# Optimization experiments

Hardware: AMD Instinct MI355X
Metric: run time of the kernel (lower is better)

## Reference

```python
import jax, jax.numpy as jnp
import numpy as np
from jax import lax

N, CIN, COUT, T, V = 32, 64, 128, 256, 25
IC = COUT // 4
EPS = 1e-5


def setup_inputs() -> dict:
    key = jax.random.key(0)
    ks = jax.random.split(key, 16)
    rn = lambda k, shape, s=0.05: jax.random.normal(k, shape, jnp.float32) * s
    inp = {
        'x': jax.random.normal(ks[0], (N, CIN, T, V), jnp.float32),
        'A': rn(ks[1], (V, V), 0.2),
        'w1': rn(ks[2], (IC, CIN)), 'b1': rn(ks[3], (IC,), 0.01),
        'w2': rn(ks[4], (IC, CIN)), 'b2': rn(ks[5], (IC,), 0.01),
        'w3': rn(ks[6], (COUT, CIN)), 'b3': rn(ks[7], (COUT,), 0.01),
        'w4': rn(ks[8], (COUT, CIN)), 'b4': rn(ks[9], (COUT,), 0.01),
        'bn1_g': jnp.ones((COUT,)), 'bn1_b': jnp.zeros((COUT,)),
        'bn1_m': rn(ks[10], (COUT,), 0.1), 'bn1_v': jnp.ones((COUT,)),
        'wt': rn(ks[11], (COUT, COUT, 9, 1)), 'bt': rn(ks[12], (COUT,), 0.01),
        'bn2_g': jnp.ones((COUT,)), 'bn2_b': jnp.zeros((COUT,)),
        'bn2_m': rn(ks[13], (COUT,), 0.1), 'bn2_v': jnp.ones((COUT,)),
        'wr': rn(ks[14], (COUT, CIN)), 'br': rn(ks[15], (COUT,), 0.01),
        'bnr_g': jnp.ones((COUT,)), 'bnr_b': jnp.zeros((COUT,)),
        'bnr_m': jnp.zeros((COUT,)), 'bnr_v': jnp.ones((COUT,)),
    }
    return inp


def _conv1x1(x, w, b):
    # 1x1 Conv2d over (T,V): pure channel mix. x: [N,C,T,V], w: [O,C]
    return jnp.einsum('oc,nctv->notv', w, x) + b[None, :, None, None]


def _bn(x, g, b, m, v):
    # BatchNorm2d in eval mode (running stats)
    scale = g / jnp.sqrt(v + EPS)
    return x * scale[None, :, None, None] + (b - m * scale)[None, :, None, None]


def _forward(x, A, w1, b1, w2, b2, w3, b3, w4, b4,
             bn1_g, bn1_b, bn1_m, bn1_v, wt, bt,
             bn2_g, bn2_b, bn2_m, bn2_v, wr, br,
             bnr_g, bnr_b, bnr_m, bnr_v):
    n, _, t, v = x.shape
    cout = w3.shape[0]
    ic = cout // 4
    x1 = _conv1x1(x, w1, b1).mean(axis=2)  # [N,IC,V]
    x2 = _conv1x1(x, w2, b2).mean(axis=2)  # [N,IC,V]
    a = jax.nn.softmax(x1[..., :, None] - x2[..., None, :], axis=-1)  # [N,IC,V,V]
    x3 = _conv1x1(x, w3, b3).reshape(n, 4, ic, t, v)
    y = jnp.einsum('ncuv,nmctv->nmctu', a, x3).reshape(n, cout, t, v)
    y = y + jnp.einsum('uv,nctv->nctu', A, _conv1x1(x, w4, b4))
    # tcn: BN -> ReLU -> Conv2d (9,1) pad (4,0) -> BN
    y = jax.nn.relu(_bn(y, bn1_g, bn1_b, bn1_m, bn1_v))
    y = lax.conv_general_dilated(
        y, wt, window_strides=(1, 1), padding=[(4, 4), (0, 0)],
        dimension_numbers=('NCHW', 'OIHW', 'NCHW')) + bt[None, :, None, None]
    y = _bn(y, bn2_g, bn2_b, bn2_m, bn2_v)
    # residual branch (in_channels != out_channels): 1x1 conv + BN
    res = _bn(_conv1x1(x, wr, br), bnr_g, bnr_b, bnr_m, bnr_v)
    return jax.nn.relu(y + res)


def reference(x, A, w1, b1, w2, b2, w3, b3, w4, b4,
              bn1_g, bn1_b, bn1_m, bn1_v, wt, bt,
              bn2_g, bn2_b, bn2_m, bn2_v, wr, br,
              bnr_g, bnr_b, bnr_m, bnr_v):
    return _forward(x, A, w1, b1, w2, b2, w3, b3, w4, b4,
                    bn1_g, bn1_b, bn1_m, bn1_v, wt, bt,
                    bn2_g, bn2_b, bn2_m, bn2_v, wr, br,
                    bnr_g, bnr_b, bnr_m, bnr_v)
```

## Files before the change

kernel.cpp:

```cpp
#include <hip/hip_runtime.h>
#include <hip/hip_bf16.h>

typedef unsigned short u16;
typedef unsigned int u32;
typedef unsigned long long u64;
typedef __attribute__((ext_vector_type(8))) short short8;
typedef __attribute__((ext_vector_type(4))) float f32x4;

#define DI __device__ __forceinline__

DI float b2f(u16 v){ u32 u = ((u32)v) << 16; float f; __builtin_memcpy(&f, &u, 4); return f; }
DI u16 f2bu(float f){ __hip_bfloat16 h = __float2bfloat16(f); u16 u; __builtin_memcpy(&u, &h, 2); return u; }

DI void gll16(const u16* g, u16* l){
  __builtin_amdgcn_global_load_lds((const __attribute__((address_space(1))) void*)g,
                                   (__attribute__((address_space(3))) void*)l, 16, 0, 0);
}

__global__ __launch_bounds__(256) void kprep(const float* __restrict__ x, u16* __restrict__ xT){
  __shared__ u16 tile[128*72];
  const int xb = blockIdx.x, n = blockIdx.y, tid = threadIdx.x;
  const int x0 = xb*128;
  const int ci = tid>>2, part = tid&3;
  const float* src = x + ((size_t)(n*64+ci))*6400 + x0 + part*32;
  #pragma unroll
  for (int i=0;i<8;i++){
    float4 f = ((const float4*)src)[i];
    const int col = part*32 + i*4;
    tile[(col+0)*72+ci] = f2bu(f.x);
    tile[(col+1)*72+ci] = f2bu(f.y);
    tile[(col+2)*72+ci] = f2bu(f.z);
    tile[(col+3)*72+ci] = f2bu(f.w);
  }
  __syncthreads();
  const int row = tid>>1, half = tid&1;
  short8* dst = (short8*)(xT + ((size_t)n*6400 + x0 + row)*64 + half*32);
  const short8* s8 = (const short8*)(tile + row*72 + half*32);
  #pragma unroll
  for (int i=0;i<4;i++) dst[i] = s8[i];
}

__global__ __launch_bounds__(256) void kzero(float* __restrict__ xm){
  const int i = blockIdx.x*1024 + threadIdx.x*4;
  float4 z = {0.f,0.f,0.f,0.f};
  *(float4*)(xm + i) = z;
}

__global__ __launch_bounds__(256) void kmean(const u16* __restrict__ xT, float* __restrict__ xm){
  __shared__ float part[4][1600];
  const int seg = blockIdx.x, n = blockIdx.y, tid = threadIdx.x;
  const int tg = tid>>6, c = tid&63;
  float acc[25];
  #pragma unroll
  for (int v=0;v<25;v++) acc[v]=0.f;
  for (int t = seg*32 + tg; t < seg*32 + 32; t += 4){
    const u16* base = xT + ((size_t)n*6400 + t*25)*64 + c;
    #pragma unroll
    for (int v=0;v<25;v++) acc[v] += b2f(base[v*64]);
  }
  #pragma unroll
  for (int v=0;v<25;v++) part[tg][v*64+c] = acc[v];
  __syncthreads();
  for (int idx = tid; idx < 1600; idx += 256){
    const int v = idx>>6, cc = idx&63;
    const float m = part[0][idx]+part[1][idx]+part[2][idx]+part[3][idx];
    atomicAdd(&xm[(n*64+cc)*25+v], m*(1.f/256.f));
  }
}

__global__ __launch_bounds__(64) void kp(const float* __restrict__ xm, const float* __restrict__ w2,
                                         const float* __restrict__ b2p, const float* __restrict__ Ab,
                                         float* __restrict__ p, float* __restrict__ rsA){
  const int c = blockIdx.x, n = blockIdx.y, lane = threadIdx.x;
  __shared__ float sc[32];
  __shared__ float red[2];
  float neg = 0.f;
  if (lane < 25){
    float acc = b2p[c];
    for (int k = 0; k < 64; k++) acc += w2[c*64 + k] * xm[(n*64 + k)*25 + lane];
    neg = -acc;
    sc[lane] = neg;
  }
  __syncthreads();
  if (lane == 0){
    float m = sc[0];
    for (int i = 1; i < 25; i++) m = fmaxf(m, sc[i]);
    red[0] = m;
  }
  __syncthreads();
  float e = 0.f;
  if (lane < 25){ e = expf(neg - red[0]); sc[lane] = e; }
  __syncthreads();
  if (lane == 0){
    float ssum = 0.f;
    for (int i = 0; i < 25; i++) ssum += sc[i];
    red[1] = ssum;
  }
  __syncthreads();
  if (lane < 25) p[(n*32 + c)*25 + lane] = e / red[1];
  if (n == 0 && c == 0 && lane < 25){
    float r = 0.f;
    for (int v = 0; v < 25; v++) r += Ab[lane*25 + v];
    rsA[lane] = r;
  }
}

__global__ __launch_bounds__(256) void kxa(const u16* __restrict__ xT, const float* __restrict__ Ab,
                                           u16* __restrict__ xA){
  __shared__ float xl[200*68];
  __shared__ float al[625];
  const int tc = blockIdx.x, n = blockIdx.y, tid = threadIdx.x;
  const int x0t = tc * 200;
  for (int i = tid; i < 625; i += 256) al[i] = Ab[i];
  for (int idx = tid; idx < 1600; idx += 256){
    const int r = idx>>3, i = idx&7;
    short8 v = *(const short8*)(xT + ((size_t)n*6400 + x0t + r)*64 + i*8);
    float* dst = xl + r*68 + i*8;
    #pragma unroll
    for (int e=0;e<8;e++) dst[e] = b2f((u16)v[e]);
  }
  __syncthreads();
  if (tid < 200){
    const int t_ = tid / 25, u = tid % 25;
    float acc[64];
    #pragma unroll
    for (int k = 0; k < 64; k++) acc[k] = 0.f;
    const float* arow = al + u*25;
    for (int v = 0; v < 25; v++){
      const float a = arow[v];
      const float* xr = xl + (t_*25 + v)*68;
      #pragma unroll
      for (int k = 0; k < 64; k++) acc[k] += a * xr[k];
    }
    u16* dst = xA + ((size_t)n*6400 + x0t + tid)*64;
    #pragma unroll
    for (int k = 0; k < 64; k += 4){
      u64 pk = (u64)f2bu(acc[k]) | ((u64)f2bu(acc[k+1])<<16)
             | ((u64)f2bu(acc[k+2])<<32) | ((u64)f2bu(acc[k+3])<<48);
      *(u64*)(dst + k) = pk;
    }
  }
}

__global__ __launch_bounds__(256) void kwt(const float* __restrict__ wt, u16* __restrict__ wtb){
  const int o = blockIdx.x*256 + threadIdx.x;
  const int dt = o >> 14, rem = o & 16383;
  wtb[o] = f2bu(wt[rem*9 + dt]);
}

__global__ __launch_bounds__(256) void kwr(const float* __restrict__ wrw, const float* __restrict__ g2,
      const float* __restrict__ v2, const float* __restrict__ gr, const float* __restrict__ vr,
      const float* __restrict__ w3, const float* __restrict__ w4,
      const float* __restrict__ bt, const float* __restrict__ bb2, const float* __restrict__ m2,
      const float* __restrict__ bbr, const float* __restrict__ mr, const float* __restrict__ brb,
      u16* __restrict__ wrb, u16* __restrict__ w3b, u16* __restrict__ w4b,
      float* __restrict__ e0, float* __restrict__ e1){
  const int b = blockIdx.x, tid = threadIdx.x;
  if (b < 32){
    const int o = b*256 + tid;
    const int co = o >> 6;
    const float E0 = g2[co]*rsqrtf(v2[co]+1e-5f);
    const float R0 = gr[co]*rsqrtf(vr[co]+1e-5f);
    wrb[o] = f2bu(wrw[o]*R0/E0);
  } else if (b < 64){
    const int o = (b-32)*256 + tid;
    w3b[o] = f2bu(w3[o]);
  } else if (b < 96){
    const int o = (b-64)*256 + tid;
    w4b[o] = f2bu(w4[o]);
  } else if (tid < 128){
    const float scv2 = g2[tid]*rsqrtf(v2[tid]+1e-5f);
    const float scvr = gr[tid]*rsqrtf(vr[tid]+1e-5f);
    e0[tid] = scv2;
    e1[tid] = scv2*bt[tid] + bb2[tid] - m2[tid]*scv2
            + (bbr[tid] - mr[tid]*scvr + scvr*brb[tid]);
  }
}

__global__ __launch_bounds__(256) void khpad(u16* __restrict__ h){
  const int n = blockIdx.x, side = blockIdx.y, tid = threadIdx.x;
  short8* base = (short8*)(h + ((size_t)n*6600 + (side ? 6500 : 0))*128);
  short8 z = {0,0,0,0,0,0,0,0};
  for (int i = tid; i < 1600; i += 256) base[i] = z;
}

__global__ __launch_bounds__(256) void ks(const u16* __restrict__ xT, const u16* __restrict__ w3b,
                                          const float* __restrict__ p, float* __restrict__ s){
  __shared__ __align__(16) char smem[53248];
  __shared__ float pL[800];
  u16* aL = (u16*)smem;
  u16* bL = (u16*)(smem + 18432);
  float* z3 = (float*)smem;
  const int xb = blockIdx.x, n = blockIdx.y, tid = threadIdx.x;
  const int x0 = xb*100, t0 = xb*4;
  const int row = tid >> 1, half = tid & 1;
  {
    short8* dst = (short8*)(aL + row*72 + half*32);
    const short8* src = (const short8*)(w3b + row*64 + half*32);
    #pragma unroll
    for (int i=0;i<4;i++) dst[i] = src[i];
  }
  {
    short8* dst = (short8*)(bL + row*72 + half*32);
    if (row < 100){
      const short8* src = (const short8*)(xT + ((size_t)n*6400 + x0 + row)*64 + half*32);
      #pragma unroll
      for (int i=0;i<4;i++) dst[i] = src[i];
    } else {
      short8 z = {0,0,0,0,0,0,0,0};
      #pragma unroll
      for (int i=0;i<4;i++) dst[i] = z;
    }
  }
  for (int i = tid; i < 800; i += 256) pL[i] = p[n*800 + i];
  __syncthreads();
  const int wave = tid>>6, lane = tid&63, q = lane>>4, l = lane&15;
  const int wr = wave>>1, wc = wave&1;
  f32x4 acc[4][4];
  #pragma unroll
  for (int i=0;i<4;i++)
    #pragma unroll
    for (int j=0;j<4;j++){ f32x4 z0 = {0.f,0.f,0.f,0.f}; acc[i][j] = z0; }
  #pragma unroll
  for (int ksi = 0; ksi < 2; ksi++){
    const int kb = ksi*32 + q*8;
    short8 af[4], bf[4];
    #pragma unroll
    for (int i=0;i<4;i++) af[i] = *(const short8*)(aL + (wr*64 + i*16 + l)*72 + kb);
    #pragma unroll
    for (int j=0;j<4;j++) bf[j] = *(const short8*)(bL + (wc*64 + j*16 + l)*72 + kb);
    #pragma unroll
    for (int i=0;i<4;i++)
      #pragma unroll
      for (int j=0;j<4;j++)
        acc[i][j] = __builtin_amdgcn_mfma_f32_16x16x32_bf16(af[i], bf[j], acc[i][j], 0, 0, 0);
  }
  __syncthreads();
  #pragma unroll
  for (int i=0;i<4;i++){
    const int co0 = wr*64 + i*16 + q*4;
    #pragma unroll
    for (int j=0;j<4;j++){
      const int colx = wc*64 + j*16 + l;
      if (colx < 100){
        #pragma unroll
        for (int r=0;r<4;r++) z3[(co0 + r)*104 + colx] = acc[i][j][r];
      }
    }
  }
  __syncthreads();
  for (int idx = tid; idx < 512; idx += 256){
    const int co = idx >> 2, tt = idx & 3;
    const float* zr = z3 + co*104 + tt*25;
    const float* pr = pL + (co & 31)*25;
    float acc2 = 0.f;
    #pragma unroll
    for (int v=0; v<25; v++) acc2 += zr[v]*pr[v];
    s[((size_t)n*128 + co)*256 + t0 + tt] = acc2;
  }
}

__global__ __launch_bounds__(256) void ky(const u16* __restrict__ xA, const u16* __restrict__ w4b,
      const float* __restrict__ s, const float* __restrict__ b3, const float* __restrict__ b4,
      const float* __restrict__ g1, const float* __restrict__ bb1, const float* __restrict__ m1,
      const float* __restrict__ v1, const float* __restrict__ rsA, u16* __restrict__ h){
  __shared__ __align__(16) u16 aL[128*72];
  __shared__ __align__(16) u16 bL[128*72];
  __shared__ float A0[128], A1[128], A2[128];
  __shared__ float sF[1024];
  __shared__ float rs[32];
  const int xb = blockIdx.x, n = blockIdx.y, tid = threadIdx.x;
  const int x0 = xb*128, tlo = x0/25;
  const int row = tid >> 1, half = tid & 1;
  {
    short8* dst = (short8*)(aL + row*72 + half*32);
    const short8* src = (const short8*)(w4b + row*64 + half*32);
    #pragma unroll
    for (int i=0;i<4;i++) dst[i] = src[i];
  }
  {
    const short8* src = (const short8*)(xA + ((size_t)n*6400 + x0 + row)*64 + half*32);
    short8* dst = (short8*)(bL + row*72 + half*32);
    #pragma unroll
    for (int i=0;i<4;i++) dst[i] = src[i];
  }
  if (tid < 128){
    const float scv = g1[tid] * rsqrtf(v1[tid] + 1e-5f);
    A0[tid] = scv;
    A1[tid] = scv * b4[tid];
    A2[tid] = bb1[tid] - m1[tid] * scv;
  }
  if (tid < 32) rs[tid] = (tid < 25) ? rsA[tid] : 0.f;
  __syncthreads();
  for (int idx = tid; idx < 1024; idx += 256){
    const int co = idx >> 3, tt = idx & 7;
    const int t = tlo + tt;
    const float sv = (t < 256) ? s[((size_t)n*128 + co)*256 + t] : 0.f;
    sF[idx] = A0[co] * (sv + b3[co]) + A2[co];
  }
  const int wave = tid>>6, lane = tid&63, q = lane>>4, l = lane&15;
  const int wr = wave>>1, wc = wave&1;
  f32x4 acc[4][4];
  #pragma unroll
  for (int i=0;i<4;i++)
    #pragma unroll
    for (int j=0;j<4;j++){ f32x4 z0 = {0.f,0.f,0.f,0.f}; acc[i][j] = z0; }
  #pragma unroll
  for (int ksi = 0; ksi < 2; ksi++){
    const int kb = ksi*32 + q*8;
    short8 af[4], bf[4];
    #pragma unroll
    for (int i=0;i<4;i++) af[i] = *(const short8*)(aL + (wr*64 + i*16 + l)*72 + kb);
    #pragma unroll
    for (int j=0;j<4;j++) bf[j] = *(const short8*)(bL + (wc*64 + j*16 + l)*72 + kb);
    #pragma unroll
    for (int i=0;i<4;i++)
      #pragma unroll
      for (int j=0;j<4;j++)
        acc[i][j] = __builtin_amdgcn_mfma_f32_16x16x32_bf16(af[i], bf[j], acc[i][j], 0, 0, 0);
  }
  __syncthreads();
  #pragma unroll
  for (int i=0;i<4;i++){
    const int co0 = wr*64 + i*16 + q*4;
    #pragma unroll
    for (int j=0;j<4;j++){
      const int colx = wc*64 + j*16 + l;
      const int xg = x0 + colx;
      const int u = xg % 25, tt = xg/25 - tlo;
      const float rsu = rs[u];
      u64 pk = 0;
      #pragma unroll
      for (int r=0;r<4;r++){
        const int co = co0 + r;
        float y = A0[co]*acc[i][j][r] + A1[co]*rsu + sF[co*8 + tt];
        y = fmaxf(y, 0.f);
        pk |= ((u64)f2bu(y)) << (16*r);
      }
      *(u64*)(h + ((size_t)n*6600 + xg + 100)*128 + co0) = pk;
    }
  }
}

__global__ __launch_bounds__(512, 2) void ktcn(const u16* __restrict__ h, const u16* __restrict__ wtb,
      const u16* __restrict__ wrb, const u16* __restrict__ xT,
      const float* __restrict__ e0g, const float* __restrict__ e1g,
      float* __restrict__ out){
  __shared__ __align__(16) char smem[149504];
  u16* hW = (u16*)smem;
  u16* Ab0 = (u16*)(smem + 83968);
  u16* Ab1 = (u16*)(smem + 116736);
  const int xb = blockIdx.x, n = blockIdx.y, tid = threadIdx.x;
  const int x0 = xb*128;
  const int wave = tid>>6, lane = tid&63, q = lane>>4, l = lane&15;
  const int wr2 = wave>>2, wc = wave&3;
  const u16* hbase = h + ((size_t)n*6600 + x0)*128;
  const u16* xtb = xT + ((size_t)n*6400 + x0)*64;

  f32x4 e0r[4], e1r[4];
  #pragma unroll
  for (int i=0;i<4;i++){
    const int co0 = wr2*64 + i*16 + q*4;
    e0r[i] = *(const f32x4*)(e0g + co0);
    e1r[i] = *(const f32x4*)(e1g + co0);
  }

  #pragma unroll
  for (int it = 0; it < 4; ++it){
    const int ci = it*512 + tid;
    const int r = ci >> 4, c = ci & 15;
    gll16(hbase + r*128 + ((c ^ (r & 15))<<3), hW + ((it*512 + wave*64)<<3));
  }
  #pragma unroll
  for (int it = 0; it < 4; ++it){
    const int ci = it*512 + tid;
    const int r = ci >> 4, c = ci & 15;
    gll16(wtb + r*128 + ((c ^ (r & 15))<<3), Ab0 + ((it*512 + wave*64)<<3));
  }
  #pragma unroll
  for (int it = 0; it < 4; ++it){
    const int ci = it*512 + tid;
    const int r = ci >> 4, c = ci & 15;
    gll16(wtb + 16384 + r*128 + ((c ^ (r & 15))<<3), Ab1 + ((it*512 + wave*64)<<3));
  }
  #pragma unroll
  for (int it = 4; it < 6; ++it){
    const int ci = it*512 + tid;
    const int r = ci >> 4, c = ci & 15;
    gll16(hbase + r*128 + ((c ^ (r & 15))<<3), hW + ((it*512 + wave*64)<<3));
  }

  f32x4 acc[4][2];
  #pragma unroll
  for (int i=0;i<4;i++)
    #pragma unroll
    for (int j=0;j<2;j++){ f32x4 z0 = {0.f,0.f,0.f,0.f}; acc[i][j] = z0; }

  asm volatile("s_waitcnt vmcnt(6) lgkmcnt(0)" ::: "memory");
  __builtin_amdgcn_s_barrier();
  __builtin_amdgcn_sched_barrier(0);

  #pragma unroll 1
  for (int dt = 0; dt <= 9; ++dt){
    if (dt >= 1 && dt <= 7){
      const u16* gA = wtb + (dt+1)*16384;
      u16* dA = ((dt+1) & 1) ? Ab1 : Ab0;
      #pragma unroll
      for (int it = 0; it < 4; ++it){
        const int ci = it*512 + tid;
        const int r = ci >> 4, c = ci & 15;
        gll16(gA + r*128 + ((c ^ (r & 15))<<3), dA + ((it*512 + wave*64)<<3));
      }
    } else if (dt == 8){
      #pragma unroll
      for (int it = 0; it < 2; ++it){
        const int ci = it*512 + tid;
        const int r = ci >> 3, c = ci & 7;
        gll16(wrb + r*64 + ((c ^ (r & 7))<<3), Ab1 + ((it*512 + wave*64)<<3));
      }
      #pragma unroll
      for (int it = 0; it < 2; ++it){
        const int ci = it*512 + tid;
        const int r = ci >> 3, c = ci & 7;
        gll16(xtb + r*64 + ((c ^ (r & 7))<<3), Ab1 + 8192 + ((it*512 + wave*64)<<3));
      }
    }
    if (dt >= 1 && dt <= 4){
      const int it = 5 + dt;
      const int ci = it*512 + tid;
      const int r = ci >> 4, c = ci & 15;
      gll16(hbase + r*128 + ((c ^ (r & 15))<<3), hW + ((it*512 + wave*64)<<3));
      if (dt == 4 && tid < 128){
        const int ci2 = 5120 + tid;
        const int r2 = ci2 >> 4, c2 = ci2 & 15;
        gll16(hbase + r2*128 + ((c2 ^ (r2 & 15))<<3), hW + ((5120 + wave*64)<<3));
      }
    }
    if (dt < 9){
      const u16* A = (dt & 1) ? Ab1 : Ab0;
      #pragma unroll
      for (int ksi = 0; ksi < 4; ksi++){
        const int c0 = ksi*4 + q;
        short8 af[4], bf[2];
        #pragma unroll
        for (int i=0;i<4;i++){
          const int r = wr2*64 + i*16 + l;
          af[i] = *(const short8*)(A + (((r<<4) + (c0 ^ (r & 15)))<<3));
        }
        #pragma unroll
        for (int j=0;j<2;j++){
          const int r = dt*25 + wc*32 + j*16 + l;
          bf[j] = *(const short8*)(hW + (((r<<4) + (c0 ^ (r & 15)))<<3));
        }
        #pragma unroll
        for (int i=0;i<4;i++)
          #pragma unroll
          for (int j=0;j<2;j++)
            acc[i][j] = __builtin_amdgcn_mfma_f32_16x16x32_bf16(af[i], bf[j], acc[i][j], 0, 0, 0);
      }
    } else {
      const u16* A = Ab1;
      const u16* B = Ab1 + 8192;
      #pragma unroll
      for (int ksi = 0; ksi < 2; ksi++){
        const int c0 = ksi*4 + q;
        short8 af[4], bf[2];
        #pragma unroll
        for (int i=0;i<4;i++){
          const int r = wr2*64 + i*16 + l;
          af[i] = *(const short8*)(A + (((r<<3) + (c0 ^ (r & 7)))<<3));
        }
        #pragma unroll
        for (int j=0;j<2;j++){
          const int r = wc*32 + j*16 + l;
          bf[j] = *(const short8*)(B + (((r<<3) + (c0 ^ (r & 7)))<<3));
        }
        #pragma unroll
        for (int i=0;i<4;i++)
          #pragma unroll
          for (int j=0;j<2;j++)
            acc[i][j] = __builtin_amdgcn_mfma_f32_16x16x32_bf16(af[i], bf[j], acc[i][j], 0, 0, 0);
      }
    }
    if (dt < 9){
      if (dt <= 4){
        asm volatile("s_waitcnt vmcnt(1) lgkmcnt(0)" ::: "memory");
        __builtin_amdgcn_s_barrier();
        __builtin_amdgcn_sched_barrier(0);
      } else {
        __syncthreads();
      }
    }
  }

  #pragma unroll
  for (int i=0;i<4;i++){
    const int co0 = wr2*64 + i*16 + q*4;
    #pragma unroll
    for (int j=0;j<2;j++){
      const int colx = wc*32 + j*16 + l;
      #pragma unroll
      for (int r=0;r<4;r++){
        const float yv = e0r[i][r]*acc[i][j][r] + e1r[i][r];
        out[((size_t)n*128 + co0 + r)*6400 + x0 + colx] = fmaxf(yv, 0.f);
      }
    }
  }
}

extern "C" void kernel_launch(void* const* d_in, const int* in_sizes, int n_in,
                              void* d_out, int out_size, void* d_ws, size_t ws_size,
                              hipStream_t stream){
  const float* x   = (const float*)d_in[0];
  const float* Ab  = (const float*)d_in[1];
  const float* w2  = (const float*)d_in[4];
  const float* b2p = (const float*)d_in[5];
  const float* w3  = (const float*)d_in[6];
  const float* b3  = (const float*)d_in[7];
  const float* w4  = (const float*)d_in[8];
  const float* b4  = (const float*)d_in[9];
  const float* g1  = (const float*)d_in[10];
  const float* bb1 = (const float*)d_in[11];
  const float* m1  = (const float*)d_in[12];
  const float* v1  = (const float*)d_in[13];
  const float* wt  = (const float*)d_in[14];
  const float* bt  = (const float*)d_in[15];
  const float* g2  = (const float*)d_in[16];
  const float* bb2 = (const float*)d_in[17];
  const float* m2  = (const float*)d_in[18];
  const float* v2  = (const float*)d_in[19];
  const float* wrw = (const float*)d_in[20];
  const float* brb = (const float*)d_in[21];
  const float* gr  = (const float*)d_in[22];
  const float* bbr = (const float*)d_in[23];
  const float* mr  = (const float*)d_in[24];
  const float* vr  = (const float*)d_in[25];
  float* out = (float*)d_out;

  char* ws = (char*)d_ws;
  float* xm  = (float*)(ws);
  float* p   = (float*)(ws + 204800);
  float* rsA = (float*)(ws + 307200);
  float* s   = (float*)(ws + 307712);
  u16* xT    = (u16*)(ws + 4502016);
  u16* xA    = (u16*)(ws + 30716416);
  u16* h     = (u16*)(ws + 56930816);
  u16* wtb   = (u16*)(ws + 110998016);
  u16* wrb   = (u16*)(ws + 111292928);
  u16* w3b   = (u16*)(ws + 111309312);
  u16* w4b   = (u16*)(ws + 111325696);
  float* e0  = (float*)(ws + 111342080);
  float* e1  = (float*)(ws + 111342592);

  kprep<<<dim3(50,32), 256, 0, stream>>>(x, xT);
  kzero<<<50, 256, 0, stream>>>(xm);
  kmean<<<dim3(8,32), 256, 0, stream>>>(xT, xm);
  kp<<<dim3(32,32), 64, 0, stream>>>(xm, w2, b2p, Ab, p, rsA);
  kxa<<<dim3(32,32), 256, 0, stream>>>(xT, Ab, xA);
  kwt<<<576, 256, 0, stream>>>(wt, wtb);
  kwr<<<97, 256, 0, stream>>>(wrw, g2, v2, gr, vr, w3, w4, bt, bb2, m2, bbr, mr, brb,
                              wrb, w3b, w4b, e0, e1);
  khpad<<<dim3(32,2), 256, 0, stream>>>(h);
  ks<<<dim3(64,32), 256, 0, stream>>>(xT, w3b, p, s);
  ky<<<dim3(50,32), 256, 0, stream>>>(xA, w4b, s, b3, b4, g1, bb1, m1, v1, rsA, h);
  ktcn<<<dim3(50,32), 512, 0, stream>>>(h, wtb, wrb, xT, e0, e1, out);
}
```

Before: 408.6 us.

## Merge setup kernels and fuse input transpose with adjacency mixing

Collapses the zeroing, weight conversion, BN folding and padding kernels into a single multi-role launch. It also fuses the fp32-to-bf16 transpose with the A-matrix mixing, so xA is computed from fp32 x held in LDS instead of re-reading xT. This removes several launches and one pass over xT. In exchange, the transpose load now uses scalar strided fp32 reads into LDS instead of float4 loads, and xA is built from unrounded fp32 inputs, which slightly changes its numerics.

```diff
diff --git a/kernel.cpp b/kernel.cpp
--- a/kernel.cpp
+++ b/kernel.cpp
@@ -17,33 +17,91 @@
                                    (__attribute__((address_space(3))) void*)l, 16, 0, 0);
 }
 
-__global__ __launch_bounds__(256) void kprep(const float* __restrict__ x, u16* __restrict__ xT){
-  __shared__ u16 tile[128*72];
-  const int xb = blockIdx.x, n = blockIdx.y, tid = threadIdx.x;
-  const int x0 = xb*128;
-  const int ci = tid>>2, part = tid&3;
-  const float* src = x + ((size_t)(n*64+ci))*6400 + x0 + part*32;
-  #pragma unroll
-  for (int i=0;i<8;i++){
-    float4 f = ((const float4*)src)[i];
-    const int col = part*32 + i*4;
-    tile[(col+0)*72+ci] = f2bu(f.x);
-    tile[(col+1)*72+ci] = f2bu(f.y);
-    tile[(col+2)*72+ci] = f2bu(f.z);
-    tile[(col+3)*72+ci] = f2bu(f.w);
-  }
-  __syncthreads();
-  const int row = tid>>1, half = tid&1;
-  short8* dst = (short8*)(xT + ((size_t)n*6400 + x0 + row)*64 + half*32);
-  const short8* s8 = (const short8*)(tile + row*72 + half*32);
-  #pragma unroll
-  for (int i=0;i<4;i++) dst[i] = s8[i];
-}
-
-__global__ __launch_bounds__(256) void kzero(float* __restrict__ xm){
-  const int i = blockIdx.x*1024 + threadIdx.x*4;
-  float4 z = {0.f,0.f,0.f,0.f};
-  *(float4*)(xm + i) = z;
+__global__ __launch_bounds__(256) void kaux(const float* __restrict__ wt, const float* __restrict__ wrw,
+      const float* __restrict__ g2, const float* __restrict__ v2,
+      const float* __restrict__ gr, const float* __restrict__ vr,
+      const float* __restrict__ w3, const float* __restrict__ w4,
+      const float* __restrict__ bt, const float* __restrict__ bb2, const float* __restrict__ m2,
+      const float* __restrict__ bbr, const float* __restrict__ mr, const float* __restrict__ brb,
+      float* __restrict__ xm, u16* __restrict__ wtb, u16* __restrict__ wrb,
+      u16* __restrict__ w3b, u16* __restrict__ w4b,
+      float* __restrict__ e0, float* __restrict__ e1, u16* __restrict__ h){
+  const int b = blockIdx.x, tid = threadIdx.x;
+  if (b < 50){
+    const int i = b*1024 + tid*4;
+    float4 z = {0.f,0.f,0.f,0.f};
+    *(float4*)(xm + i) = z;
+  } else if (b < 626){
+    const int o = (b-50)*256 + tid;
+    const int dt = o >> 14, rem = o & 16383;
+    wtb[o] = f2bu(wt[rem*9 + dt]);
+  } else if (b < 658){
+    const int o = (b-626)*256 + tid;
+    const int co = o >> 6;
+    const float E0 = g2[co]*rsqrtf(v2[co]+1e-5f);
+    const float R0 = gr[co]*rsqrtf(vr[co]+1e-5f);
+    wrb[o] = f2bu(wrw[o]*R0/E0);
+  } else if (b < 690){
+    const int o = (b-658)*256 + tid;
+    w3b[o] = f2bu(w3[o]);
+  } else if (b < 722){
+    const int o = (b-690)*256 + tid;
+    w4b[o] = f2bu(w4[o]);
+  } else if (b < 786){
+    const int j = b - 722, n = j >> 1, side = j & 1;
+    short8* base = (short8*)(h + ((size_t)n*6600 + (side ? 6500 : 0))*128);
+    short8 z = {0,0,0,0,0,0,0,0};
+    for (int i = tid; i < 1600; i += 256) base[i] = z;
+  } else {
+    if (tid < 128){
+      const float scv2 = g2[tid]*rsqrtf(v2[tid]+1e-5f);
+      const float scvr = gr[tid]*rsqrtf(vr[tid]+1e-5f);
+      e0[tid] = scv2;
+      e1[tid] = scv2*bt[tid] + bb2[tid] - m2[tid]*scv2
+              + (bbr[tid] - mr[tid]*scvr + scvr*brb[tid]);
+    }
+  }
+}
+
+__global__ __launch_bounds__(256) void kprep2(const float* __restrict__ x, const float* __restrict__ Ab,
+                                              u16* __restrict__ xT, u16* __restrict__ xA){
+  __shared__ float xl[200*68];
+  __shared__ float al[625];
+  const int tc = blockIdx.x, n = blockIdx.y, tid = threadIdx.x;
+  const int x0t = tc * 200;
+  for (int i = tid; i < 625; i += 256) al[i] = Ab[i];
+  for (int idx = tid; idx < 12800; idx += 256){
+    const int ci = idx / 200, col = idx - ci*200;
+    xl[col*68 + ci] = x[((size_t)(n*64+ci))*6400 + x0t + col];
+  }
+  __syncthreads();
+  for (int idx = tid; idx < 3200; idx += 256){
+    const int r = idx >> 4, k4 = (idx & 15) << 2;
+    const float* src = xl + r*68 + k4;
+    u64 pk = (u64)f2bu(src[0]) | ((u64)f2bu(src[1])<<16)
+           | ((u64)f2bu(src[2])<<32) | ((u64)f2bu(src[3])<<48);
+    *(u64*)(xT + ((size_t)n*6400 + x0t + r)*64 + k4) = pk;
+  }
+  if (tid < 200){
+    const int t_ = tid / 25, u = tid % 25;
+    float acc[64];
+    #pragma unroll
+    for (int k = 0; k < 64; k++) acc[k] = 0.f;
+    const float* arow = al + u*25;
+    for (int v = 0; v < 25; v++){
+      const float a = arow[v];
+      const float* xr = xl + (t_*25 + v)*68;
+      #pragma unroll
+      for (int k = 0; k < 64; k++) acc[k] += a * xr[k];
+    }
+    u16* dst = xA + ((size_t)n*6400 + x0t + tid)*64;
+    #pragma unroll
+    for (int k = 0; k < 64; k += 4){
+      u64 pk = (u64)f2bu(acc[k]) | ((u64)f2bu(acc[k+1])<<16)
+             | ((u64)f2bu(acc[k+2])<<32) | ((u64)f2bu(acc[k+3])<<48);
+      *(u64*)(dst + k) = pk;
+    }
+  }
 }
 
 __global__ __launch_bounds__(256) void kmean(const u16* __restrict__ xT, float* __restrict__ xm){
@@ -103,85 +161,6 @@
     for (int v = 0; v < 25; v++) r += Ab[lane*25 + v];
     rsA[lane] = r;
   }
-}
-
-__global__ __launch_bounds__(256) void kxa(const u16* __restrict__ xT, const float* __restrict__ Ab,
-                                           u16* __restrict__ xA){
-  __shared__ float xl[200*68];
-  __shared__ float al[625];
-  const int tc = blockIdx.x, n = blockIdx.y, tid = threadIdx.x;
-  const int x0t = tc * 200;
-  for (int i = tid; i < 625; i += 256) al[i] = Ab[i];
-  for (int idx = tid; idx < 1600; idx += 256){
-    const int r = idx>>3, i = idx&7;
-    short8 v = *(const short8*)(xT + ((size_t)n*6400 + x0t + r)*64 + i*8);
-    float* dst = xl + r*68 + i*8;
-    #pragma unroll
-    for (int e=0;e<8;e++) dst[e] = b2f((u16)v[e]);
-  }
-  __syncthreads();
-  if (tid < 200){
-    const int t_ = tid / 25, u = tid % 25;
-    float acc[64];
-    #pragma unroll
-    for (int k = 0; k < 64; k++) acc[k] = 0.f;
-    const float* arow = al + u*25;
-    for (int v = 0; v < 25; v++){
-      const float a = arow[v];
-      const float* xr = xl + (t_*25 + v)*68;
-      #pragma unroll
-      for (int k = 0; k < 64; k++) acc[k] += a * xr[k];
-    }
-    u16* dst = xA + ((size_t)n*6400 + x0t + tid)*64;
-    #pragma unroll
-    for (int k = 0; k < 64; k += 4){
-      u64 pk = (u64)f2bu(acc[k]) | ((u64)f2bu(acc[k+1])<<16)
-             | ((u64)f2bu(acc[k+2])<<32) | ((u64)f2bu(acc[k+3])<<48);
-      *(u64*)(dst + k) = pk;
-    }
-  }
-}
-
-__global__ __launch_bounds__(256) void kwt(const float* __restrict__ wt, u16* __restrict__ wtb){
-  const int o = blockIdx.x*256 + threadIdx.x;
-  const int dt = o >> 14, rem = o & 16383;
-  wtb[o] = f2bu(wt[rem*9 + dt]);
-}
-
-__global__ __launch_bounds__(256) void kwr(const float* __restrict__ wrw, const float* __restrict__ g2,
-      const float* __restrict__ v2, const float* __restrict__ gr, const float* __restrict__ vr,
-      const float* __restrict__ w3, const float* __restrict__ w4,
-      const float* __restrict__ bt, const float* __restrict__ bb2, const float* __restrict__ m2,
-      const float* __restrict__ bbr, const float* __restrict__ mr, const float* __restrict__ brb,
-      u16* __restrict__ wrb, u16* __restrict__ w3b, u16* __restrict__ w4b,
-      float* __restrict__ e0, float* __restrict__ e1){
-  const int b = blockIdx.x, tid = threadIdx.x;
-  if (b < 32){
-    const int o = b*256 + tid;
-    const int co = o >> 6;
-    const float E0 = g2[co]*rsqrtf(v2[co]+1e-5f);
-    const float R0 = gr[co]*rsqrtf(vr[co]+1e-5f);
-    wrb[o] = f2bu(wrw[o]*R0/E0);
-  } else if (b < 64){
-    const int o = (b-32)*256 + tid;
-    w3b[o] = f2bu(w3[o]);
-  } else if (b < 96){
-    const int o = (b-64)*256 + tid;
-    w4b[o] = f2bu(w4[o]);
-  } else if (tid < 128){
-    const float scv2 = g2[tid]*rsqrtf(v2[tid]+1e-5f);
-    const float scvr = gr[tid]*rsqrtf(vr[tid]+1e-5f);
-    e0[tid] = scv2;
-    e1[tid] = scv2*bt[tid] + bb2[tid] - m2[tid]*scv2
-            + (bbr[tid] - mr[tid]*scvr + scvr*brb[tid]);
-  }
-}
-
-__global__ __launch_bounds__(256) void khpad(u16* __restrict__ h){
-  const int n = blockIdx.x, side = blockIdx.y, tid = threadIdx.x;
-  short8* base = (short8*)(h + ((size_t)n*6600 + (side ? 6500 : 0))*128);
-  short8 z = {0,0,0,0,0,0,0,0};
-  for (int i = tid; i < 1600; i += 256) base[i] = z;
 }
 
 __global__ __launch_bounds__(256) void ks(const u16* __restrict__ xT, const u16* __restrict__ w3b,
@@ -552,15 +531,11 @@
   float* e0  = (float*)(ws + 111342080);
   float* e1  = (float*)(ws + 111342592);
 
-  kprep<<<dim3(50,32), 256, 0, stream>>>(x, xT);
-  kzero<<<50, 256, 0, stream>>>(xm);
+  kaux<<<787, 256, 0, stream>>>(wt, wrw, g2, v2, gr, vr, w3, w4, bt, bb2, m2, bbr, mr, brb,
+                                xm, wtb, wrb, w3b, w4b, e0, e1, h);
+  kprep2<<<dim3(32,32), 256, 0, stream>>>(x, Ab, xT, xA);
   kmean<<<dim3(8,32), 256, 0, stream>>>(xT, xm);
   kp<<<dim3(32,32), 64, 0, stream>>>(xm, w2, b2p, Ab, p, rsA);
-  kxa<<<dim3(32,32), 256, 0, stream>>>(xT, Ab, xA);
-  kwt<<<576, 256, 0, stream>>>(wt, wtb);
-  kwr<<<97, 256, 0, stream>>>(wrw, g2, v2, gr, vr, w3, w4, bt, bb2, m2, bbr, mr, brb,
-                              wrb, w3b, w4b, e0, e1);
-  khpad<<<dim3(32,2), 256, 0, stream>>>(h);
   ks<<<dim3(64,32), 256, 0, stream>>>(xT, w3b, p, s);
   ky<<<dim3(50,32), 256, 0, stream>>>(xA, w4b, s, b3, b4, g1, bb1, m1, v1, rsA, h);
   ktcn<<<dim3(50,32), 512, 0, stream>>>(h, wtb, wrb, xT, e0, e1, out);
```

After: 397.8 us. -2.6%, faster.
